# Kernel tuning notes

Measured on AMD Instinct MI355X. Metric: run time of the kernel, lower is better.

The kernel has to match this reference:

```python
import jax, jax.numpy as jnp
import numpy as np

N = 20000   # nodes
E = 320000  # edges (before self-loops)
D = 128     # input_dim
HID = 128   # hidden_dim
HEADS = 4


def _ln(x, g, b):
    mu = x.mean(-1, keepdims=True)
    var = x.var(-1, keepdims=True)
    return (x - mu) * jax.lax.rsqrt(var + 1e-5) * g + b


def _seg_softmax(a, seg, n):
    # numerically-stable segment softmax over destination nodes
    m = jax.ops.segment_max(a, seg, num_segments=n)
    e = jnp.exp(a - m[seg])
    s = jax.ops.segment_sum(e, seg, num_segments=n)
    return e / (s[seg] + 1e-16)


def _gatv2(x, src, dst, Wl, bl, Wr, br, att, bias, heads, c, concat, n):
    # GATv2Conv: e_ij = att . leaky_relu(xl[j] + xr[i]); softmax over i's neighbors
    xl = (x @ Wl + bl).reshape(n, heads, c)
    xr = (x @ Wr + br).reshape(n, heads, c)
    e = jax.nn.leaky_relu(xl[src] + xr[dst], 0.2)        # [E, H, C]
    a = _seg_softmax(jnp.einsum('ehc,hc->eh', e, att), dst, n)
    out = jax.ops.segment_sum(xl[src] * a[:, :, None], dst, num_segments=n)
    out = out.reshape(n, heads * c) if concat else out.mean(1)
    return out + bias


def setup_inputs() -> dict:
    key = jax.random.key(0)
    ks = iter(jax.random.split(key, 64))
    def nrm(shape, s=0.05):
        return jax.random.normal(next(ks), shape, jnp.float32) * s
    d = {}
    d['x'] = jax.random.normal(next(ks), (N, D), jnp.float32)
    d['edge_index'] = jax.random.randint(next(ks), (2, E), 0, N)
    d['fn_g'] = jnp.ones(D); d['fn_b'] = jnp.zeros(D)
    d['W_in'] = nrm((D, HID)); d['b_in'] = jnp.zeros(HID)
    d['Wl1'] = nrm((HID, HEADS * HID)); d['bl1'] = jnp.zeros(HEADS * HID)
    d['Wr1'] = nrm((HID, HEADS * HID)); d['br1'] = jnp.zeros(HEADS * HID)
    d['att1'] = nrm((HEADS, HID)); d['bg1'] = jnp.zeros(HEADS * HID)
    d['Wl2'] = nrm((HEADS * HID, HID)); d['bl2'] = jnp.zeros(HID)
    d['Wr2'] = nrm((HEADS * HID, HID)); d['br2'] = jnp.zeros(HID)
    d['att2'] = nrm((1, HID)); d['bg2'] = jnp.zeros(HID)
    d['ln1_g'] = jnp.ones(HEADS * HID); d['ln1_b'] = jnp.zeros(HEADS * HID)
    d['ln2_g'] = jnp.ones(HID); d['ln2_b'] = jnp.zeros(HID)
    for p in ['rf', 'cf', 'kf']:
        d['W' + p] = nrm((HID, HID)); d['b' + p] = jnp.zeros(HID)
        d[p + '_g'] = jnp.ones(HID); d[p + '_b'] = jnp.zeros(HID)
    d['Wr1h'] = nrm((HID, HID // 2)); d['br1h'] = jnp.zeros(HID // 2)
    d['Wr2h'] = nrm((HID // 2, HID // 4)); d['br2h'] = jnp.zeros(HID // 4)
    d['Wr3h'] = nrm((HID // 4, 1)); d['br3h'] = jnp.zeros(1)
    d['Wc1h'] = nrm((HID, HID // 2)); d['bc1h'] = jnp.zeros(HID // 2)
    d['Wc2h'] = nrm((HID // 2, 2)); d['bc2h'] = jnp.zeros(2)
    d['Wk1h'] = nrm((HID, HID // 2)); d['bk1h'] = jnp.zeros(HID // 2)
    d['Wk2h'] = nrm((HID // 2, 1)); d['bk2h'] = jnp.zeros(1)
    return d


def reference(x, edge_index, fn_g, fn_b, W_in, b_in,
              Wl1, bl1, Wr1, br1, att1, bg1,
              Wl2, bl2, Wr2, br2, att2, bg2,
              ln1_g, ln1_b, ln2_g, ln2_b,
              Wrf, brf, rf_g, rf_b, Wcf, bcf, cf_g, cf_b, Wkf, bkf, kf_g, kf_b,
              Wr1h, br1h, Wr2h, br2h, Wr3h, br3h,
              Wc1h, bc1h, Wc2h, bc2h, Wk1h, bk1h, Wk2h, bk2h):
    n = x.shape[0]
    h = _ln(x, fn_g, fn_b)
    h = jax.nn.relu(h @ W_in + b_in)
    loops = jnp.arange(n)
    src = jnp.concatenate([edge_index[0], loops])
    dst = jnp.concatenate([edge_index[1], loops])
    h = _gatv2(h, src, dst, Wl1, bl1, Wr1, br1, att1, bg1, HEADS, HID, True, n)
    h = jax.nn.elu(_ln(h, ln1_g, ln1_b))
    h = _gatv2(h, src, dst, Wl2, bl2, Wr2, br2, att2, bg2, 1, HID, False, n)
    emb = jax.nn.elu(_ln(h, ln2_g, ln2_b))
    def feat(W, b, g, bb):
        return jax.nn.relu(_ln(emb @ W + b, g, bb))
    rf = feat(Wrf, brf, rf_g, rf_b)
    cf = feat(Wcf, bcf, cf_g, cf_b)
    kf = feat(Wkf, bkf, kf_g, kf_b)
    returns_pred = jnp.tanh(jax.nn.relu(jax.nn.relu(rf @ Wr1h + br1h) @ Wr2h + br2h) @ Wr3h + br3h) * 0.1
    movement_pred = jax.nn.relu(cf @ Wc1h + bc1h) @ Wc2h + bc2h
    ranking_scores = jax.nn.sigmoid(jax.nn.relu(kf @ Wk1h + bk1h) @ Wk2h + bk2h)
    return (returns_pred, movement_pred, ranking_scores, emb)
```

## Files before the change

kernel.cpp:

```cpp
#include <hip/hip_runtime.h>
#include <cmath>

#define DEV __device__ __forceinline__
#define LOG2E 1.44269504088896340736f

typedef __attribute__((ext_vector_type(8))) short short8v;
typedef __attribute__((ext_vector_type(4))) float f32x4;
typedef __attribute__((ext_vector_type(2))) float f32x2;

DEV float lrelu(float v) { return fmaxf(v, 0.2f * v); }
DEV float elu(float v) { return v > 0.f ? v : expm1f(v); }
DEV float plo(unsigned u) { return __uint_as_float(u << 16); }
DEV float phi(unsigned u) { return __uint_as_float(u & 0xffff0000u); }
DEV f32x2 pk2(unsigned u) {
  return f32x2{__uint_as_float(u << 16), __uint_as_float(u & 0xffff0000u)};
}
DEV unsigned short f2bf(float f) {
  unsigned u = __float_as_uint(f);
  unsigned r = (u + 0x7fffu + ((u >> 16) & 1u)) >> 16;
  return (unsigned short)r;
}
DEV unsigned packbf(float a, float b) {
  return (unsigned)f2bf(a) | ((unsigned)f2bf(b) << 16);
}

__global__ void k_count(const int* __restrict__ ei, int* __restrict__ counts,
                        int E0, int ET) {
  int e = blockIdx.x * 256 + threadIdx.x;
  if (e >= ET) return;
  int dst = (e < E0) ? ei[E0 + e] : (e - E0);
  atomicAdd(&counts[dst], 1);
}

__global__ __launch_bounds__(1024) void k_scan2(const int* __restrict__ counts,
                                                int* __restrict__ offs, int n) {
  int t = threadIdx.x;
  int ch = (n + 1023) >> 10;
  int beg = t * ch, end = min(beg + ch, n);
  int loc = 0;
  for (int i = beg; i < end; ++i) loc += counts[i];
  int lane = t & 63, w = t >> 6;
  int v = loc;
#pragma unroll
  for (int m = 1; m < 64; m <<= 1) {
    int u = __shfl_up(v, m);
    if (lane >= m) v += u;
  }
  __shared__ int wsum[16], wpre[16];
  if (lane == 63) wsum[w] = v;
  __syncthreads();
  if (t < 16) {
    int p = 0;
    for (int i = 0; i < t; ++i) p += wsum[i];
    wpre[t] = p;
  }
  __syncthreads();
  int run = wpre[w] + v - loc;
  for (int i = beg; i < end; ++i) { offs[i] = run; run += counts[i]; }
  if (beg < n && end == n) offs[n] = run;
}

__global__ void k_scatter(const int* __restrict__ ei, const int* __restrict__ offs,
                          int* __restrict__ cursor, int* __restrict__ src_s,
                          int E0, int ET) {
  int e = blockIdx.x * 256 + threadIdx.x;
  if (e >= ET) return;
  int src, dst;
  if (e < E0) { src = ei[e]; dst = ei[E0 + e]; }
  else        { src = e - E0; dst = e - E0; }
  int pos = offs[dst] + atomicAdd(&cursor[dst], 1);
  src_s[pos] = src;
}

DEV void pack_one(const float* __restrict__ W, unsigned short* __restrict__ Wp,
                  int K, int N, int idx) {
  if (idx >= K * N) return;
  int j = idx & 7, l = (idx >> 3) & 63, r = idx >> 9;
  int KB = K / 32;
  int tile = r / KB, kb = r - tile * KB;
  int k = kb * 32 + (l >> 4) * 8 + j;
  int col = tile * 16 + (l & 15);
  Wp[idx] = f2bf(W[(size_t)k * N + col]);
}

__global__ void k_pack_all(const float* w0, const float* w1, const float* w2,
                           const float* w3, const float* w4, const float* w5,
                           const float* w6, const float* w7,
                           unsigned short* p0, unsigned short* p1, unsigned short* p2,
                           unsigned short* p3, unsigned short* p4, unsigned short* p5,
                           unsigned short* p6, unsigned short* p7,
                           const float* bl1, const float* br1, float* bcatA,
                           const float* bl2, const float* br2, float* bcatB) {
  int idx = blockIdx.x * 256 + threadIdx.x;
  pack_one(w0, p0, 128, 128, idx);
  pack_one(w1, p1, 128, 512, idx);
  pack_one(w2, p2, 128, 512, idx);
  pack_one(w3, p3, 512, 128, idx);
  pack_one(w4, p4, 512, 128, idx);
  pack_one(w5, p5, 128, 128, idx);
  pack_one(w6, p6, 128, 128, idx);
  pack_one(w7, p7, 128, 128, idx);
  if (idx < 512) bcatA[idx] = bl1[idx];
  else if (idx < 1024) bcatA[idx] = br1[idx - 512];
  if (idx < 128) bcatB[idx] = bl2[idx];
  else if (idx < 256) bcatB[idx] = br2[idx - 128];
}

DEV float bd1_val(const float* Wr, const float* Wc, const float* Wk, int k, int col) {
  int blk = col >> 6;
  if ((k >> 7) != blk) return 0.f;
  const float* W = (blk == 0) ? Wr : (blk == 1) ? Wc : Wk;
  return W[(k & 127) * 64 + (col & 63)];
}
DEV float bd2_val(const float* Wr2, const float* Wc2, const float* Wk2, int k, int col) {
  if (col < 32) return (k < 64) ? Wr2[k * 32 + col] : 0.f;
  if (col < 34) return (k >= 64 && k < 128) ? Wc2[(k - 64) * 2 + (col - 32)] : 0.f;
  if (col == 34) return (k >= 128) ? Wk2[k - 128] : 0.f;
  return 0.f;
}

__global__ void k_pack_heads(const float* Wr1, const float* Wc1, const float* Wk1,
                             const float* Wr2, const float* Wc2, const float* Wk2,
                             const float* br1, const float* bc1, const float* bk1,
                             const float* br2, const float* bc2, const float* bk2,
                             unsigned short* P1, unsigned short* P2,
                             float* bh1, float* bh2) {
  int idx = blockIdx.x * 256 + threadIdx.x;
  if (idx < 384 * 192) {
    int j = idx & 7, l = (idx >> 3) & 63, r = idx >> 9;
    const int KB = 12;
    int tile = r / KB, kb = r - tile * KB;
    int k = kb * 32 + (l >> 4) * 8 + j;
    int col = tile * 16 + (l & 15);
    P1[idx] = f2bf(bd1_val(Wr1, Wc1, Wk1, k, col));
  }
  if (idx < 192 * 64) {
    int j = idx & 7, l = (idx >> 3) & 63, r = idx >> 9;
    const int KB = 6;
    int tile = r / KB, kb = r - tile * KB;
    int k = kb * 32 + (l >> 4) * 8 + j;
    int col = tile * 16 + (l & 15);
    P2[idx] = f2bf(bd2_val(Wr2, Wc2, Wk2, k, col));
  }
  if (idx < 192) bh1[idx] = (idx < 64) ? br1[idx] : (idx < 128) ? bc1[idx - 64] : bk1[idx - 128];
  if (idx < 64)
    bh2[idx] = (idx < 32) ? br2[idx] : (idx < 34) ? bc2[idx - 32] : (idx == 34) ? bk2[0] : 0.f;
}

template<int K, int N, int RT, int ACT, bool OF32, bool OB16>
__global__ __launch_bounds__(256) void k_mfma(const unsigned short* __restrict__ A,
                                              const unsigned short* __restrict__ Wp,
                                              const float* __restrict__ bias,
                                              float* __restrict__ Cf,
                                              unsigned short* __restrict__ Cb) {
  constexpr int KB = K / 32;
  constexpr int TPW = N / 64;
  __shared__ short As[RT * KB * 64 * 8];
  int row0 = blockIdx.x * (16 * RT);
  int t = threadIdx.x, lane = t & 63, w = t >> 6;
  for (int idx = t; idx < RT * KB * 64; idx += 256) {
    int r = idx / (KB * 64), rem = idx - r * (KB * 64);
    int kb = rem >> 6, l = rem & 63;
    const short8v* sp = reinterpret_cast<const short8v*>(
        A + (size_t)(row0 + r * 16 + (l & 15)) * K + kb * 32 + (l >> 4) * 8);
    reinterpret_cast<short8v*>(As)[idx] = *sp;
  }
  __syncthreads();
  f32x4 acc[RT][TPW];
#pragma unroll
  for (int r = 0; r < RT; ++r)
#pragma unroll
    for (int j = 0; j < TPW; ++j) acc[r][j] = f32x4{0.f, 0.f, 0.f, 0.f};
  const short8v* Bp = reinterpret_cast<const short8v*>(Wp);
  for (int kb = 0; kb < KB; ++kb) {
    short8v a[RT];
#pragma unroll
    for (int r = 0; r < RT; ++r)
      a[r] = reinterpret_cast<const short8v*>(As)[(r * KB + kb) * 64 + lane];
#pragma unroll
    for (int j = 0; j < TPW; ++j) {
      int tile = w * TPW + j;
      short8v b = Bp[(tile * KB + kb) * 64 + lane];
#pragma unroll
      for (int r = 0; r < RT; ++r)
        acc[r][j] = __builtin_amdgcn_mfma_f32_16x16x32_bf16(a[r], b, acc[r][j], 0, 0, 0);
    }
  }
#pragma unroll
  for (int j = 0; j < TPW; ++j) {
    int col = (w * TPW + j) * 16 + (lane & 15);
    float bs = bias[col];
#pragma unroll
    for (int rt = 0; rt < RT; ++rt)
#pragma unroll
      for (int r = 0; r < 4; ++r) {
        int row = row0 + rt * 16 + (lane >> 4) * 4 + r;
        float v = acc[rt][j][r] + bs;
        if (ACT == 1) v = fmaxf(v, 0.f);
        if (OF32) Cf[(size_t)row * N + col] = v;
        if (OB16) Cb[(size_t)row * N + col] = f2bf(v);
      }
  }
}

template<int C, int ACT, bool OUT16>
__global__ void k_ln(const float* in, void* out, const float* g, const float* b) {
  constexpr int T = (C < 256) ? C : 256;
  constexpr int EPT = C / T;
  int row = blockIdx.x, t = threadIdx.x;
  const float* ip = in + (size_t)row * C;
  float v[EPT];
  float s = 0.f, s2 = 0.f;
#pragma unroll
  for (int e = 0; e < EPT; ++e) { float xv = ip[t + e * T]; v[e] = xv; s += xv; s2 += xv * xv; }
#pragma unroll
  for (int m = 1; m <= 32; m <<= 1) { s += __shfl_xor(s, m); s2 += __shfl_xor(s2, m); }
  __shared__ float w1s[2], w2s[2];
  if (T > 64) {
    if ((t & 63) == 0) { w1s[t >> 6] = s; w2s[t >> 6] = s2; }
    __syncthreads();
    s = w1s[0] + w1s[1];
    s2 = w2s[0] + w2s[1];
  }
  float mu = s * (1.0f / C);
  float var = s2 * (1.0f / C) - mu * mu;
  float rs = rsqrtf(var + 1e-5f);
#pragma unroll
  for (int e = 0; e < EPT; ++e) {
    int c = t + e * T;
    float y = (v[e] - mu) * rs * g[c] + b[c];
    if (ACT == 1) y = fmaxf(y, 0.f);
    if (ACT == 2) y = elu(y);
    if (OUT16) ((unsigned short*)out)[(size_t)row * C + c] = f2bf(y);
    else       ((float*)out)[(size_t)row * C + c] = y;
  }
}

__global__ __launch_bounds__(256) void k_gat1(const int* __restrict__ offs,
                                              const int* __restrict__ src_s,
                                              const uint4* __restrict__ xlr4,
                                              const float* __restrict__ att,
                                              const float* __restrict__ bg,
                                              const float* __restrict__ lg,
                                              const float* __restrict__ lb,
                                              uint4* __restrict__ out4,
                                              int M) {
  int w = threadIdx.x >> 6, lane = threadIdx.x & 63;
  int n = blockIdx.x * 4 + w;
  if (n >= M) return;
  int st = offs[n], en = offs[n + 1];
  int cb = lane * 8;
  uint4 ur = xlr4[(unsigned)n * 128u + 64u + lane];
  f32x2 xr[4] = {pk2(ur.x), pk2(ur.y), pk2(ur.z), pk2(ur.w)};
  f32x2 atv[4];
  {
    const float4* atp = reinterpret_cast<const float4*>(att + cb);
    float4 a0 = atp[0], a1 = atp[1];
    atv[0] = f32x2{a0.x, a0.y} * LOG2E;
    atv[1] = f32x2{a0.z, a0.w} * LOG2E;
    atv[2] = f32x2{a1.x, a1.y} * LOG2E;
    atv[3] = f32x2{a1.z, a1.w} * LOG2E;
  }
  float s = 0.f;
  f32x2 acc[4] = {f32x2{0.f, 0.f}, f32x2{0.f, 0.f}, f32x2{0.f, 0.f}, f32x2{0.f, 0.f}};
  uint4 u0 = xlr4[(unsigned)src_s[st] * 128u + lane];
  uint4 u1 = xlr4[(unsigned)src_s[st + 1 < en ? st + 1 : st] * 128u + lane];
  for (int i = st; i < en; ++i) {
    uint4 uc = u0;
    u0 = u1;
    int nx = (i + 2 < en) ? i + 2 : en - 1;
    u1 = xlr4[(unsigned)src_s[nx] * 128u + lane];
    f32x2 xv[4] = {pk2(uc.x), pk2(uc.y), pk2(uc.z), pk2(uc.w)};
    f32x2 ps = f32x2{0.f, 0.f};
#pragma unroll
    for (int k = 0; k < 4; ++k) {
      f32x2 t = xv[k] + xr[k];
      f32x2 lr = __builtin_elementwise_max(t, 0.2f * t);
      ps += atv[k] * lr;
    }
    float p = ps.x + ps.y;
    p += __shfl_xor(p, 1);
    p += __shfl_xor(p, 2);
    p += __shfl_xor(p, 4);
    p += __shfl_xor(p, 8);
    float we = exp2f(fminf(p, 80.f));
    s += we;
#pragma unroll
    for (int k = 0; k < 4; ++k) acc[k] += we * xv[k];
  }
  float inv = 1.0f / (s + 1e-16f);
  float v[8];
  float s1 = 0.f, s2 = 0.f;
#pragma unroll
  for (int k = 0; k < 4; ++k) {
    v[2 * k]     = fmaf(acc[k].x, inv, bg[cb + 2 * k]);
    v[2 * k + 1] = fmaf(acc[k].y, inv, bg[cb + 2 * k + 1]);
    s1 += v[2 * k] + v[2 * k + 1];
    s2 += v[2 * k] * v[2 * k] + v[2 * k + 1] * v[2 * k + 1];
  }
#pragma unroll
  for (int mm = 1; mm <= 32; mm <<= 1) { s1 += __shfl_xor(s1, mm); s2 += __shfl_xor(s2, mm); }
  float mu = s1 * (1.0f / 512.0f);
  float var = s2 * (1.0f / 512.0f) - mu * mu;
  float rsd = rsqrtf(var + 1e-5f);
  float y[8];
#pragma unroll
  for (int k = 0; k < 8; ++k)
    y[k] = elu((v[k] - mu) * rsd * lg[cb + k] + lb[cb + k]);
  uint4 o;
  o.x = packbf(y[0], y[1]); o.y = packbf(y[2], y[3]);
  o.z = packbf(y[4], y[5]); o.w = packbf(y[6], y[7]);
  out4[(unsigned)n * 64u + lane] = o;
}

__global__ __launch_bounds__(256) void k_gat2(const int* __restrict__ offs,
                                              const int* __restrict__ src_s,
                                              const uint4* __restrict__ xlr4,
                                              const float* __restrict__ att,
                                              const float* __restrict__ bg,
                                              const float* __restrict__ lg,
                                              const float* __restrict__ lb,
                                              float* __restrict__ emb,
                                              uint4* __restrict__ embh4,
                                              int M) {
  int w = threadIdx.x >> 6, lane = threadIdx.x & 63;
  int n = blockIdx.x * 4 + w;
  if (n >= M) return;
  int st = offs[n], en = offs[n + 1];
  int g = lane >> 4, l16 = lane & 15;
  int cb = l16 * 8;
  uint4 ur = xlr4[(unsigned)n * 32u + 16u + l16];
  f32x2 xr[4] = {pk2(ur.x), pk2(ur.y), pk2(ur.z), pk2(ur.w)};
  f32x2 atv[4];
  {
    const float4* atp = reinterpret_cast<const float4*>(att + cb);
    float4 a0 = atp[0], a1 = atp[1];
    atv[0] = f32x2{a0.x, a0.y} * LOG2E;
    atv[1] = f32x2{a0.z, a0.w} * LOG2E;
    atv[2] = f32x2{a1.x, a1.y} * LOG2E;
    atv[3] = f32x2{a1.z, a1.w} * LOG2E;
  }
  float s = 0.f;
  f32x2 acc[4] = {f32x2{0.f, 0.f}, f32x2{0.f, 0.f}, f32x2{0.f, 0.f}, f32x2{0.f, 0.f}};
  int e0 = st + g, e1 = st + 4 + g;
  uint4 u0 = xlr4[(unsigned)src_s[e0 < en ? e0 : en - 1] * 32u + l16];
  uint4 u1 = xlr4[(unsigned)src_s[e1 < en ? e1 : en - 1] * 32u + l16];
  for (int i = st; i < en; i += 4) {
    int e = i + g;
    uint4 uc = u0;
    u0 = u1;
    int e2 = i + 8 + g;
    u1 = xlr4[(unsigned)src_s[e2 < en ? e2 : en - 1] * 32u + l16];
    f32x2 xv[4] = {pk2(uc.x), pk2(uc.y), pk2(uc.z), pk2(uc.w)};
    f32x2 ps = f32x2{0.f, 0.f};
#pragma unroll
    for (int k = 0; k < 4; ++k) {
      f32x2 t = xv[k] + xr[k];
      f32x2 lr = __builtin_elementwise_max(t, 0.2f * t);
      ps += atv[k] * lr;
    }
    float p = ps.x + ps.y;
    p += __shfl_xor(p, 1);
    p += __shfl_xor(p, 2);
    p += __shfl_xor(p, 4);
    p += __shfl_xor(p, 8);
    float we = (e < en) ? exp2f(fminf(p, 80.f)) : 0.f;
    s += we;
#pragma unroll
    for (int k = 0; k < 4; ++k) acc[k] += we * xv[k];
  }
#pragma unroll
  for (int d = 16; d < 64; d <<= 1) {
    s += __shfl_xor(s, d);
#pragma unroll
    for (int k = 0; k < 4; ++k) {
      acc[k].x += __shfl_xor(acc[k].x, d);
      acc[k].y += __shfl_xor(acc[k].y, d);
    }
  }
  float inv = 1.0f / (s + 1e-16f);
  float v[8];
  float s1 = 0.f, s2 = 0.f;
#pragma unroll
  for (int k = 0; k < 4; ++k) {
    v[2 * k]     = fmaf(acc[k].x, inv, bg[cb + 2 * k]);
    v[2 * k + 1] = fmaf(acc[k].y, inv, bg[cb + 2 * k + 1]);
    s1 += v[2 * k] + v[2 * k + 1];
    s2 += v[2 * k] * v[2 * k] + v[2 * k + 1] * v[2 * k + 1];
  }
#pragma unroll
  for (int mm = 1; mm <= 32; mm <<= 1) { s1 += __shfl_xor(s1, mm); s2 += __shfl_xor(s2, mm); }
  float mu = s1 * (1.0f / 512.0f);
  float var = s2 * (1.0f / 512.0f) - mu * mu;
  float rsd = rsqrtf(var + 1e-5f);
  if (g == 0) {
    float y[8];
#pragma unroll
    for (int k = 0; k < 8; ++k)
      y[k] = elu((v[k] - mu) * rsd * lg[cb + k] + lb[cb + k]);
    float* ep = emb + (size_t)n * 128 + cb;
    *reinterpret_cast<float4*>(ep)     = float4{y[0], y[1], y[2], y[3]};
    *reinterpret_cast<float4*>(ep + 4) = float4{y[4], y[5], y[6], y[7]};
    uint4 o;
    o.x = packbf(y[0], y[1]); o.y = packbf(y[2], y[3]);
    o.z = packbf(y[4], y[5]); o.w = packbf(y[6], y[7]);
    embh4[(unsigned)n * 16u + l16] = o;
  }
}

__global__ __launch_bounds__(256) void k_branch(const unsigned short* __restrict__ A,
    const unsigned short* __restrict__ Wp,
    const float* __restrict__ b0, const float* __restrict__ b1s, const float* __restrict__ b2s,
    const float* __restrict__ g0, const float* __restrict__ gb0,
    const float* __restrict__ g1, const float* __restrict__ gb1,
    const float* __restrict__ g2, const float* __restrict__ gb2,
    unsigned* __restrict__ ffh) {
  constexpr int KB = 4, TPW = 6;
  __shared__ short As[KB * 64 * 8];
  __shared__ float Cs[16 * 384];
  int row0 = blockIdx.x * 16;
  int t = threadIdx.x, lane = t & 63, w = t >> 6;
  for (int idx = t; idx < KB * 64; idx += 256) {
    int kb = idx >> 6, l = idx & 63;
    const short8v* sp = reinterpret_cast<const short8v*>(
        A + (size_t)(row0 + (l & 15)) * 128 + kb * 32 + (l >> 4) * 8);
    reinterpret_cast<short8v*>(As)[idx] = *sp;
  }
  __syncthreads();
  f32x4 acc[TPW];
#pragma unroll
  for (int j = 0; j < TPW; ++j) acc[j] = f32x4{0.f, 0.f, 0.f, 0.f};
  const short8v* Bp = reinterpret_cast<const short8v*>(Wp);
  for (int kb = 0; kb < KB; ++kb) {
    short8v a = reinterpret_cast<const short8v*>(As)[kb * 64 + lane];
#pragma unroll
    for (int j = 0; j < TPW; ++j) {
      int tile = w * TPW + j;
      short8v b = Bp[(tile * KB + kb) * 64 + lane];
      acc[j] = __builtin_amdgcn_mfma_f32_16x16x32_bf16(a, b, acc[j], 0, 0, 0);
    }
  }
#pragma unroll
  for (int j = 0; j < TPW; ++j) {
    int col = (w * TPW + j) * 16 + (lane & 15);
    int seg = col >> 7, cl = col & 127;
    const float* bp = (seg == 0) ? b0 : (seg == 1) ? b1s : b2s;
    float bs = bp[cl];
#pragma unroll
    for (int r = 0; r < 4; ++r)
      Cs[((lane >> 4) * 4 + r) * 384 + col] = acc[j][r] + bs;
  }
  __syncthreads();
  int row = t >> 4, l16 = t & 15;
#pragma unroll
  for (int seg = 0; seg < 3; ++seg) {
    float v[8];
    float s = 0.f, s2 = 0.f;
    int base = row * 384 + seg * 128 + l16 * 8;
#pragma unroll
    for (int k = 0; k < 8; ++k) { v[k] = Cs[base + k]; s += v[k]; s2 += v[k] * v[k]; }
#pragma unroll
    for (int mm = 1; mm <= 8; mm <<= 1) { s += __shfl_xor(s, mm); s2 += __shfl_xor(s2, mm); }
    float mu = s * (1.0f / 128.0f);
    float var = s2 * (1.0f / 128.0f) - mu * mu;
    float rsd = rsqrtf(var + 1e-5f);
    const float* gp = (seg == 0) ? g0 : (seg == 1) ? g1 : g2;
    const float* bp = (seg == 0) ? gb0 : (seg == 1) ? gb1 : gb2;
    unsigned* op = ffh + (size_t)(row0 + row) * 192 + seg * 64 + l16 * 4;
    float y[8];
#pragma unroll
    for (int k = 0; k < 8; ++k) {
      int c = l16 * 8 + k;
      y[k] = fmaxf((v[k] - mu) * rsd * gp[c] + bp[c], 0.f);
    }
    op[0] = packbf(y[0], y[1]); op[1] = packbf(y[2], y[3]);
    op[2] = packbf(y[4], y[5]); op[3] = packbf(y[6], y[7]);
  }
}

__global__ void k_tail(const float* __restrict__ tmp,
                       const float* __restrict__ Wr3, const float* __restrict__ br3,
                       float* __restrict__ out_ret, float* __restrict__ out_mov,
                       float* __restrict__ out_rank, int M) {
  int row = blockIdx.x * 256 + threadIdx.x;
  if (row >= M) return;
  const float4* tp = reinterpret_cast<const float4*>(tmp + (size_t)row * 64);
  float4 v[9];
#pragma unroll
  for (int q = 0; q < 9; ++q) v[q] = tp[q];
  const float* tv = reinterpret_cast<const float*>(v);
  float a3 = br3[0];
#pragma unroll
  for (int k = 0; k < 32; ++k) a3 = fmaf(fmaxf(tv[k], 0.f), Wr3[k], a3);
  out_ret[row] = tanhf(a3) * 0.1f;
  out_mov[2 * row]     = tv[32];
  out_mov[2 * row + 1] = tv[33];
  out_rank[row] = 1.0f / (1.0f + expf(-tv[34]));
}

extern "C" void kernel_launch(void* const* d_in, const int* in_sizes, int n_in,
                              void* d_out, int out_size, void* d_ws, size_t ws_size,
                              hipStream_t stream) {
  const float* x     = (const float*)d_in[0];
  const int*   ei    = (const int*)  d_in[1];
  const float* fn_g  = (const float*)d_in[2];
  const float* fn_b  = (const float*)d_in[3];
  const float* W_in  = (const float*)d_in[4];
  const float* b_in  = (const float*)d_in[5];
  const float* Wl1   = (const float*)d_in[6];
  const float* bl1   = (const float*)d_in[7];
  const float* Wr1   = (const float*)d_in[8];
  const float* br1   = (const float*)d_in[9];
  const float* att1  = (const float*)d_in[10];
  const float* bg1   = (const float*)d_in[11];
  const float* Wl2   = (const float*)d_in[12];
  const float* bl2   = (const float*)d_in[13];
  const float* Wr2   = (const float*)d_in[14];
  const float* br2   = (const float*)d_in[15];
  const float* att2  = (const float*)d_in[16];
  const float* bg2   = (const float*)d_in[17];
  const float* ln1_g = (const float*)d_in[18];
  const float* ln1_b = (const float*)d_in[19];
  const float* ln2_g = (const float*)d_in[20];
  const float* ln2_b = (const float*)d_in[21];
  const float* Wrf   = (const float*)d_in[22];
  const float* brf   = (const float*)d_in[23];
  const float* rf_g  = (const float*)d_in[24];
  const float* rf_b  = (const float*)d_in[25];
  const float* Wcf   = (const float*)d_in[26];
  const float* bcf   = (const float*)d_in[27];
  const float* cf_g  = (const float*)d_in[28];
  const float* cf_b  = (const float*)d_in[29];
  const float* Wkf   = (const float*)d_in[30];
  const float* bkf   = (const float*)d_in[31];
  const float* kf_g  = (const float*)d_in[32];
  const float* kf_b  = (const float*)d_in[33];
  const float* Wr1h  = (const float*)d_in[34];
  const float* br1h  = (const float*)d_in[35];
  const float* Wr2h  = (const float*)d_in[36];
  const float* br2h  = (const float*)d_in[37];
  const float* Wr3h  = (const float*)d_in[38];
  const float* br3h  = (const float*)d_in[39];
  const float* Wc1h  = (const float*)d_in[40];
  const float* bc1h  = (const float*)d_in[41];
  const float* Wc2h  = (const float*)d_in[42];
  const float* bc2h  = (const float*)d_in[43];
  const float* Wk1h  = (const float*)d_in[44];
  const float* bk1h  = (const float*)d_in[45];
  const float* Wk2h  = (const float*)d_in[46];
  const float* bk2h  = (const float*)d_in[47];

  const int M  = in_sizes[0] / 128;
  const int E0 = in_sizes[1] / 2;
  const int ET = E0 + M;

  char* base = (char*)d_ws;
  size_t off = 0;
  auto carve = [&](size_t bytes) -> char* {
    off = (off + 255) & ~(size_t)255;
    char* p = base + off;
    off += bytes;
    return p;
  };
  const size_t B1024 = (size_t)M * 1024 * 2;
  const size_t B512 = (size_t)M * 512 * 2;
  const size_t B256 = (size_t)M * 256 * 2;
  const size_t B128 = (size_t)M * 128 * 2;
  unsigned short* hnh   = (unsigned short*)carve(B128);
  unsigned short* h0h   = (unsigned short*)carve(B128);
  unsigned short* xlr1h = (unsigned short*)carve(B1024);
  unsigned short* g1h   = (unsigned short*)carve(B512);
  unsigned short* xlr2h = (unsigned short*)carve(B256);
  unsigned short* embh  = (unsigned short*)carve(B128);
  int* src_s = (int*)carve((size_t)(ET + 8) * sizeof(int));
  int* cnt   = (int*)carve((size_t)2 * M * sizeof(int));
  int* cur   = cnt + M;
  int* offs  = (int*)carve((size_t)(M + 1) * sizeof(int));
  unsigned short* Winp = (unsigned short*)carve(128 * 128 * 2);
  unsigned short* Wl1p = (unsigned short*)carve(128 * 512 * 2);
  unsigned short* Wr1p = (unsigned short*)carve(128 * 512 * 2);
  unsigned short* Wl2p = (unsigned short*)carve(512 * 128 * 2);
  unsigned short* Wr2p = (unsigned short*)carve(512 * 128 * 2);
  unsigned short* Wtp  = (unsigned short*)carve(3 * 128 * 128 * 2);
  unsigned short* Wh1p = (unsigned short*)carve(384 * 192 * 2);
  unsigned short* Wh2p = (unsigned short*)carve(192 * 64 * 2);
  float* bcatA = (float*)carve(1024 * sizeof(float));
  float* bcatB = (float*)carve(256 * sizeof(float));
  float* bh1  = (float*)carve(192 * sizeof(float));
  float* bh2  = (float*)carve(64 * sizeof(float));
  unsigned* ffh = (unsigned*)xlr1h;
  unsigned short* h1h = xlr1h + (size_t)M * 256;
  float* tmp = (float*)g1h;
  (void)ws_size; (void)n_in; (void)out_size; (void)Wr1p; (void)Wr2p;

  hipMemsetAsync(cnt, 0, (size_t)2 * M * sizeof(int), stream);
  k_count<<<(ET + 255) / 256, 256, 0, stream>>>(ei, cnt, E0, ET);
  k_scan2<<<1, 1024, 0, stream>>>(cnt, offs, M);
  k_scatter<<<(ET + 255) / 256, 256, 0, stream>>>(ei, offs, cur, src_s, E0, ET);

  k_pack_all<<<256, 256, 0, stream>>>(W_in, Wl1, Wr1, Wl2, Wr2, Wrf, Wcf, Wkf,
                                      Winp, Wl1p, Wr1p, Wl2p, Wr2p,
                                      Wtp, Wtp + 16384, Wtp + 32768,
                                      bl1, br1, bcatA, bl2, br2, bcatB);
  k_pack_heads<<<288, 256, 0, stream>>>(Wr1h, Wc1h, Wk1h, Wr2h, Wc2h, Wk2h,
                                        br1h, bc1h, bk1h, br2h, bc2h, bk2h,
                                        Wh1p, Wh2p, bh1, bh2);

  k_ln<128, 0, true><<<M, 128, 0, stream>>>(x, hnh, fn_g, fn_b);
  k_mfma<128, 128, 2, 1, false, true><<<M / 32, 256, 0, stream>>>(hnh, Winp, b_in, nullptr, h0h);
  k_mfma<128, 1024, 2, 0, false, true><<<M / 32, 256, 0, stream>>>(h0h, Wl1p, bcatA, nullptr, xlr1h);
  k_gat1<<<(M + 3) / 4, 256, 0, stream>>>(offs, src_s, (const uint4*)xlr1h,
                                          att1, bg1, ln1_g, ln1_b, (uint4*)g1h, M);
  k_mfma<512, 256, 2, 0, false, true><<<M / 32, 256, 0, stream>>>(g1h, Wl2p, bcatB, nullptr, xlr2h);

  float* out_ret  = (float*)d_out;
  float* out_mov  = out_ret + M;
  float* out_rank = out_ret + 3 * M;
  float* emb      = out_ret + 4 * M;
  k_gat2<<<(M + 3) / 4, 256, 0, stream>>>(offs, src_s, (const uint4*)xlr2h,
                                          att2, bg2, ln2_g, ln2_b, emb, (uint4*)embh, M);

  k_branch<<<M / 16, 256, 0, stream>>>(embh, Wtp, brf, bcf, bkf,
                                       rf_g, rf_b, cf_g, cf_b, kf_g, kf_b, ffh);

  k_mfma<384, 192, 2, 1, false, true><<<M / 32, 256, 0, stream>>>(
      (const unsigned short*)ffh, Wh1p, bh1, nullptr, h1h);
  k_mfma<192, 64, 2, 0, true, false><<<M / 32, 256, 0, stream>>>(
      h1h, Wh2p, bh2, tmp, nullptr);
  k_tail<<<(M + 255) / 256, 256, 0, stream>>>(tmp, Wr3h, br3h,
                                              out_ret, out_mov, out_rank, M);
}
```

Baseline: 288.5 us.

## Split GAT1 edge loop across two wavefronts per node and deepen GAT2 prefetch

Measured after the change: 286.6 us. About the same (-0.7%).

```diff
diff --git a/kernel.cpp b/kernel.cpp
--- a/kernel.cpp
+++ b/kernel.cpp
@@ -10,8 +10,6 @@
 
 DEV float lrelu(float v) { return fmaxf(v, 0.2f * v); }
 DEV float elu(float v) { return v > 0.f ? v : expm1f(v); }
-DEV float plo(unsigned u) { return __uint_as_float(u << 16); }
-DEV float phi(unsigned u) { return __uint_as_float(u & 0xffff0000u); }
 DEV f32x2 pk2(unsigned u) {
   return f32x2{__uint_as_float(u << 16), __uint_as_float(u & 0xffff0000u)};
 }
@@ -246,12 +244,20 @@
                                               uint4* __restrict__ out4,
                                               int M) {
   int w = threadIdx.x >> 6, lane = threadIdx.x & 63;
-  int n = blockIdx.x * 4 + w;
-  if (n >= M) return;
-  int st = offs[n], en = offs[n + 1];
+  int ln_node = w >> 1;
+  int j = w & 1;
+  int n = blockIdx.x * 2 + ln_node;
+  bool active = n < M;
+  __shared__ float sm_acc[2][64][8];
+  __shared__ float sm_s[2][64];
+  int st = 0, en = 0;
+  if (active) { st = offs[n]; en = offs[n + 1]; }
   int cb = lane * 8;
-  uint4 ur = xlr4[(unsigned)n * 128u + 64u + lane];
-  f32x2 xr[4] = {pk2(ur.x), pk2(ur.y), pk2(ur.z), pk2(ur.w)};
+  f32x2 xr[4] = {f32x2{0.f,0.f}, f32x2{0.f,0.f}, f32x2{0.f,0.f}, f32x2{0.f,0.f}};
+  if (active) {
+    uint4 ur = xlr4[(unsigned)n * 128u + 64u + lane];
+    xr[0] = pk2(ur.x); xr[1] = pk2(ur.y); xr[2] = pk2(ur.z); xr[3] = pk2(ur.w);
+  }
   f32x2 atv[4];
   {
     const float4* atp = reinterpret_cast<const float4*>(att + cb);
@@ -261,32 +267,53 @@
     atv[2] = f32x2{a1.x, a1.y} * LOG2E;
     atv[3] = f32x2{a1.z, a1.w} * LOG2E;
   }
+  auto ld = [&](int i) -> uint4 {
+    int ii = (i < en) ? i : en - 1;
+    return xlr4[(unsigned)src_s[ii] * 128u + lane];
+  };
   float s = 0.f;
   f32x2 acc[4] = {f32x2{0.f, 0.f}, f32x2{0.f, 0.f}, f32x2{0.f, 0.f}, f32x2{0.f, 0.f}};
-  uint4 u0 = xlr4[(unsigned)src_s[st] * 128u + lane];
-  uint4 u1 = xlr4[(unsigned)src_s[st + 1 < en ? st + 1 : st] * 128u + lane];
-  for (int i = st; i < en; ++i) {
-    uint4 uc = u0;
-    u0 = u1;
-    int nx = (i + 2 < en) ? i + 2 : en - 1;
-    u1 = xlr4[(unsigned)src_s[nx] * 128u + lane];
-    f32x2 xv[4] = {pk2(uc.x), pk2(uc.y), pk2(uc.z), pk2(uc.w)};
-    f32x2 ps = f32x2{0.f, 0.f};
+  if (active && st + j < en) {
+    uint4 u0 = ld(st + j);
+    uint4 u1 = ld(st + j + 2);
+    for (int i = st + j; i < en; i += 2) {
+      uint4 uc = u0;
+      u0 = u1;
+      u1 = ld(i + 4);
+      f32x2 xv[4] = {pk2(uc.x), pk2(uc.y), pk2(uc.z), pk2(uc.w)};
+      f32x2 ps = f32x2{0.f, 0.f};
+#pragma unroll
+      for (int k = 0; k < 4; ++k) {
+        f32x2 t = xv[k] + xr[k];
+        f32x2 lr = __builtin_elementwise_max(t, 0.2f * t);
+        ps += atv[k] * lr;
+      }
+      float p = ps.x + ps.y;
+      p += __shfl_xor(p, 1);
+      p += __shfl_xor(p, 2);
+      p += __shfl_xor(p, 4);
+      p += __shfl_xor(p, 8);
+      float we = exp2f(fminf(p, 80.f));
+      s += we;
+#pragma unroll
+      for (int k = 0; k < 4; ++k) acc[k] += we * xv[k];
+    }
+  }
+  if (j == 1) {
+    sm_s[ln_node][lane] = s;
 #pragma unroll
     for (int k = 0; k < 4; ++k) {
-      f32x2 t = xv[k] + xr[k];
-      f32x2 lr = __builtin_elementwise_max(t, 0.2f * t);
-      ps += atv[k] * lr;
+      sm_acc[ln_node][lane][2 * k]     = acc[k].x;
+      sm_acc[ln_node][lane][2 * k + 1] = acc[k].y;
     }
-    float p = ps.x + ps.y;
-    p += __shfl_xor(p, 1);
-    p += __shfl_xor(p, 2);
-    p += __shfl_xor(p, 4);
-    p += __shfl_xor(p, 8);
-    float we = exp2f(fminf(p, 80.f));
-    s += we;
-#pragma unroll
-    for (int k = 0; k < 4; ++k) acc[k] += we * xv[k];
+  }
+  __syncthreads();
+  if (j != 0 || !active) return;
+  s += sm_s[ln_node][lane];
+#pragma unroll
+  for (int k = 0; k < 4; ++k) {
+    acc[k].x += sm_acc[ln_node][lane][2 * k];
+    acc[k].y += sm_acc[ln_node][lane][2 * k + 1];
   }
   float inv = 1.0f / (s + 1e-16f);
   float v[8];
@@ -340,17 +367,18 @@
     atv[2] = f32x2{a1.x, a1.y} * LOG2E;
     atv[3] = f32x2{a1.z, a1.w} * LOG2E;
   }
+  auto ld = [&](int jj) -> uint4 {
+    int j2 = (jj < en) ? jj : en - 1;
+    return xlr4[(unsigned)src_s[j2] * 32u + l16];
+  };
   float s = 0.f;
   f32x2 acc[4] = {f32x2{0.f, 0.f}, f32x2{0.f, 0.f}, f32x2{0.f, 0.f}, f32x2{0.f, 0.f}};
-  int e0 = st + g, e1 = st + 4 + g;
-  uint4 u0 = xlr4[(unsigned)src_s[e0 < en ? e0 : en - 1] * 32u + l16];
-  uint4 u1 = xlr4[(unsigned)src_s[e1 < en ? e1 : en - 1] * 32u + l16];
+  uint4 u0 = ld(st + g), u1 = ld(st + 4 + g), u2 = ld(st + 8 + g), u3 = ld(st + 12 + g);
   for (int i = st; i < en; i += 4) {
     int e = i + g;
     uint4 uc = u0;
-    u0 = u1;
-    int e2 = i + 8 + g;
-    u1 = xlr4[(unsigned)src_s[e2 < en ? e2 : en - 1] * 32u + l16];
+    u0 = u1; u1 = u2; u2 = u3;
+    u3 = ld(i + 16 + g);
     f32x2 xv[4] = {pk2(uc.x), pk2(uc.y), pk2(uc.z), pk2(uc.w)};
     f32x2 ps = f32x2{0.f, 0.f};
 #pragma unroll
@@ -609,7 +637,7 @@
   k_ln<128, 0, true><<<M, 128, 0, stream>>>(x, hnh, fn_g, fn_b);
   k_mfma<128, 128, 2, 1, false, true><<<M / 32, 256, 0, stream>>>(hnh, Winp, b_in, nullptr, h0h);
   k_mfma<128, 1024, 2, 0, false, true><<<M / 32, 256, 0, stream>>>(h0h, Wl1p, bcatA, nullptr, xlr1h);
-  k_gat1<<<(M + 3) / 4, 256, 0, stream>>>(offs, src_s, (const uint4*)xlr1h,
+  k_gat1<<<(M + 1) / 2, 256, 0, stream>>>(offs, src_s, (const uint4*)xlr1h,
                                           att1, bg1, ln1_g, ln1_b, (uint4*)g1h, M);
   k_mfma<512, 256, 2, 0, false, true><<<M / 32, 256, 0, stream>>>(g1h, Wl2p, bcatB, nullptr, xlr2h);
 
```
